# Optimization experiments

Measured on AMD Instinct MI355X. Metric: run time of the kernel, lower is better.

## Reference

```python
import jax, jax.numpy as jnp
import numpy as np

EMBED_DIM = 1024
NUM_HEADS = 16
HEAD_DIM = EMBED_DIM // NUM_HEADS
EXPANSION = 4
EPS = 1e-5


def setup_inputs() -> dict:
    key = jax.random.key(0)
    ks = jax.random.split(key, 8)
    D, F = EMBED_DIM, EMBED_DIM * EXPANSION
    s = lambda d: 1.0 / np.sqrt(d)
    return {
        "x": jax.random.normal(ks[0], (8, 1024, D), jnp.float32),
        "qkv_w": jax.random.normal(ks[1], (D, 3 * D), jnp.float32) * s(D),
        "qkv_b": jnp.zeros((3 * D,), jnp.float32),
        "out_w": jax.random.normal(ks[2], (D, D), jnp.float32) * s(D),
        "out_b": jnp.zeros((D,), jnp.float32),
        "ffn_w1": jax.random.normal(ks[3], (D, F), jnp.float32) * s(D),
        "ffn_b1": jnp.zeros((F,), jnp.float32),
        "ffn_w2": jax.random.normal(ks[4], (F, D), jnp.float32) * s(F),
        "ffn_b2": jnp.zeros((D,), jnp.float32),
        "ln1_g": jnp.ones((D,), jnp.float32),
        "ln1_b": jnp.zeros((D,), jnp.float32),
        "ln2_g": jnp.ones((D,), jnp.float32),
        "ln2_b": jnp.zeros((D,), jnp.float32),
    }


def _layernorm(x, g, b):
    mu = jnp.mean(x, axis=-1, keepdims=True)
    var = jnp.mean(jnp.square(x - mu), axis=-1, keepdims=True)
    return (x - mu) * jax.lax.rsqrt(var + EPS) * g + b


def reference(x, qkv_w, qkv_b, out_w, out_b, ffn_w1, ffn_b1, ffn_w2, ffn_b2,
              ln1_g, ln1_b, ln2_g, ln2_b):
    B, N, D = x.shape
    H, Hd = NUM_HEADS, HEAD_DIM
    scale = Hd ** -0.5

    residual = x
    h = _layernorm(x, ln1_g, ln1_b)
    qkv = h @ qkv_w + qkv_b                      # [B, N, 3D]
    q, k, v = jnp.split(qkv, 3, axis=-1)
    # [B, N, D] -> [B, H, N, Hd]
    reshape = lambda t: t.reshape(B, N, H, Hd).transpose(0, 2, 1, 3)
    q, k, v = reshape(q), reshape(k), reshape(v)

    attn = jnp.einsum("bhnd,bhmd->bhnm", q, k) * scale
    attn = jax.nn.softmax(attn, axis=-1)
    o = jnp.einsum("bhnm,bhmd->bhnd", attn, v)   # [B, H, N, Hd]
    o = o.transpose(0, 2, 1, 3).reshape(B, N, D)
    o = o @ out_w + out_b
    x = residual + o

    residual = x
    h = _layernorm(x, ln2_g, ln2_b)
    h = jax.nn.gelu(h @ ffn_w1 + ffn_b1, approximate=False) @ ffn_w2 + ffn_b2
    return residual + h
```

## Files before the change

kernel.cpp:

```cpp
#include <hip/hip_runtime.h>
#include <hip/hip_bf16.h>


typedef float f32x4 __attribute__((ext_vector_type(4)));
typedef float f32x16 __attribute__((ext_vector_type(16)));
typedef short bf16x8 __attribute__((ext_vector_type(8)));

#define DEV __device__ __forceinline__

DEV f32x4 mfma16(bf16x8 a, bf16x8 b, f32x4 c) {
    return __builtin_amdgcn_mfma_f32_16x16x32_bf16(a, b, c, 0, 0, 0);
}

DEV f32x16 mfma32(bf16x8 a, bf16x8 b, f32x16 c) {
    return __builtin_amdgcn_mfma_f32_32x32x16_bf16(a, b, c, 0, 0, 0);
}

DEV ushort f2bf(float f) {
    union { float f; unsigned u; } v; v.f = f;
    unsigned r = v.u + 0x7FFFu + ((v.u >> 16) & 1u);
    return (ushort)(r >> 16);
}

DEV unsigned cvtpk(float lo, float hi) {
    unsigned r;
    asm("v_cvt_pk_bf16_f32 %0, %1, %2" : "=v"(r) : "v"(lo), "v"(hi));
    return r;
}

DEV void gload_lds16(const void* g, void* l) {
    __builtin_amdgcn_global_load_lds(
        (const __attribute__((address_space(1))) void*)g,
        (__attribute__((address_space(3))) void*)l, 16, 0, 0);
}

template <int N> DEV void vmwait() {
    asm volatile("s_waitcnt vmcnt(%0)" :: "n"(N) : "memory");
}
DEV void lgkm0() {
    asm volatile("s_waitcnt lgkmcnt(0)" ::: "memory");
}

__global__ __launch_bounds__(256) void transpose_w(
    const float* __restrict__ src, ushort* __restrict__ dst, int K, int N)
{
    __shared__ float tile[32][33];
    const int n0 = blockIdx.x * 32, k0 = blockIdx.y * 32;
    const int tx = threadIdx.x, ty = threadIdx.y;
#pragma unroll
    for (int i = 0; i < 32; i += 8)
        tile[ty + i][tx] = src[(size_t)(k0 + ty + i) * N + n0 + tx];
    __syncthreads();
#pragma unroll
    for (int i = 0; i < 32; i += 8)
        dst[(size_t)(n0 + ty + i) * K + k0 + tx] = f2bf(tile[tx][ty + i]);
}

__global__ __launch_bounds__(256) void transpose_v(
    const ushort* __restrict__ qkvb, ushort* __restrict__ vt)
{
    __shared__ ushort tile[32][33];
    const int b = blockIdx.z >> 4, h = blockIdx.z & 15;
    const int n0 = blockIdx.x * 32, d0 = blockIdx.y * 32;
    const int tx = threadIdx.x, ty = threadIdx.y;
#pragma unroll
    for (int i = 0; i < 32; i += 8)
        tile[ty + i][tx] =
            qkvb[(size_t)(b * 1024 + n0 + ty + i) * 3072 + 2048 + h * 64 + d0 + tx];
    __syncthreads();
#pragma unroll
    for (int i = 0; i < 32; i += 8)
        vt[((size_t)(b * 16 + h) * 64 + d0 + ty + i) * 1024 + n0 + tx] = tile[tx][ty + i];
}

__global__ __launch_bounds__(256) void ln_bf16(
    const float* __restrict__ x, const float* __restrict__ gw,
    const float* __restrict__ bw, ushort* __restrict__ out)
{
    const int row = blockIdx.x;
    const int t = threadIdx.x;
    const float4 v = ((const float4*)(x + (size_t)row * 1024))[t];
    float s  = v.x + v.y + v.z + v.w;
    float s2 = v.x * v.x + v.y * v.y + v.z * v.z + v.w * v.w;
#pragma unroll
    for (int off = 32; off; off >>= 1) {
        s  += __shfl_xor(s, off);
        s2 += __shfl_xor(s2, off);
    }
    __shared__ float red[16];
    const int wave = t >> 6, lane = t & 63;
    if (lane == 0) { red[wave] = s; red[8 + wave] = s2; }
    __syncthreads();
    s  = red[0] + red[1] + red[2] + red[3];
    s2 = red[8] + red[9] + red[10] + red[11];
    const float mean = s * (1.0f / 1024.0f);
    const float var  = s2 * (1.0f / 1024.0f) - mean * mean;
    const float rstd = rsqrtf(var + 1e-5f);
    const float4 gv = ((const float4*)gw)[t];
    const float4 bv = ((const float4*)bw)[t];
    ushort4 o;
    o.x = f2bf((v.x - mean) * rstd * gv.x + bv.x);
    o.y = f2bf((v.y - mean) * rstd * gv.y + bv.y);
    o.z = f2bf((v.z - mean) * rstd * gv.z + bv.z);
    o.w = f2bf((v.w - mean) * rstd * gv.w + bv.w);
    ((ushort4*)out)[(size_t)row * 256 + t] = o;
}

template <int BM, int BN, int WM_, int WN_, int EPI>
__global__ __launch_bounds__(512, 2) void gemm4p(
    const ushort* __restrict__ A, const ushort* __restrict__ BT,
    const float* __restrict__ bias, const float* __restrict__ res,
    void* __restrict__ out, int M, int N, int K)
{
    constexpr int BK = 64;
    constexpr int MR = BM / WM_ / 16;
    constexpr int NR = BN / WN_ / 16;
    constexpr int MH = MR / 2;
    constexpr int CM = MH / 2;
    constexpr int LA = (BM / 2) / 64;
    constexpr int LB = (BN / 2) / 64;
    constexpr int VMN = LA + LB;
    constexpr int ABYTES = BM * BK * 2;
    constexpr int BBYTES = BN * BK * 2;

    extern __shared__ __align__(16) char smem[];
#define ASB(b) (smem + (b) * ABYTES)
#define BSB(b) (smem + 2 * ABYTES + (b) * BBYTES)

    const int tid = threadIdx.x;
    const int wave = tid >> 6, lane = tid & 63;
    const int g = lane >> 4, lr = lane & 15;
    const int wr = wave / WN_, wc = wave % WN_;
    const int akey = (lr & 7) << 4;

    const int gx = gridDim.x;
    const int nwg = gx * gridDim.y;
    int id = blockIdx.y * gx + blockIdx.x;
    id = (id & 7) * (nwg >> 3) + (id >> 3);
    const int m0 = (id / gx) * BM, n0 = (id % gx) * BN;

    const int trow = tid >> 3;
    const int tblk = (tid & 7) ^ (trow & 7);
    const ushort* pA = A  + (size_t)(m0 + trow) * K + tblk * 8;
    const ushort* pB = BT + (size_t)(n0 + trow) * K + tblk * 8;
    const int woff = wave * 1024;

#define STAGE_A(b, h, kt) do { \
    _Pragma("unroll") for (int i = 0; i < LA; ++i) \
        gload_lds16(pA + ((size_t)((h) * (BM / 2) + i * 64)) * K + (size_t)(kt) * 64, \
                    ASB(b) + (h) * (BM / 2) * 128 + i * 8192 + woff); \
} while (0)
#define STAGE_B(b, h, kt) do { \
    _Pragma("unroll") for (int i = 0; i < LB; ++i) \
        gload_lds16(pB + ((size_t)((h) * (BN / 2) + i * 64)) * K + (size_t)(kt) * 64, \
                    BSB(b) + (h) * (BN / 2) * 128 + i * 8192 + woff); \
} while (0)

    bf16x8 af[CM][2], bfr[NR][2];
    f32x4 acc[MR][NR] = {};

#define LOAD_A(b, h, cj) do { \
    const char* rb_ = ASB(b) + ((h) * (BM / 2) + wr * ((BM / 2) / WM_) \
                               + (cj) * CM * 16 + lr) * 128; \
    _Pragma("unroll") for (int cm = 0; cm < CM; ++cm) \
    _Pragma("unroll") for (int kk = 0; kk < 2; ++kk) \
        af[cm][kk] = *(const bf16x8*)(rb_ + cm * 2048 + ((kk * 64 + g * 16) ^ akey)); \
} while (0)
#define LOAD_B(b) do { \
    const char* rb_ = BSB(b) + (wc * (BN / WN_) + lr) * 128; \
    _Pragma("unroll") for (int ni = 0; ni < NR; ++ni) \
    _Pragma("unroll") for (int kk = 0; kk < 2; ++kk) \
        bfr[ni][kk] = *(const bf16x8*)(rb_ + ni * 2048 + ((kk * 64 + g * 16) ^ akey)); \
} while (0)
#define MFMA_PH(h, cj) do { \
    __builtin_amdgcn_s_setprio(1); \
    _Pragma("unroll") for (int cm = 0; cm < CM; ++cm) \
    _Pragma("unroll") for (int ni = 0; ni < NR; ++ni) \
    _Pragma("unroll") for (int kk = 0; kk < 2; ++kk) \
        acc[(h) * MH + (cj) * CM + cm][ni] = \
            mfma16(af[cm][kk], bfr[ni][kk], acc[(h) * MH + (cj) * CM + cm][ni]); \
    __builtin_amdgcn_s_setprio(0); \
} while (0)

    const int NT = K >> 6;

    STAGE_A(0, 0, 0); STAGE_A(0, 1, 0); STAGE_B(0, 0, 0); STAGE_B(0, 1, 0);
    STAGE_B(1, 0, 1);
    STAGE_A(1, 0, 1);
    vmwait<VMN>();
    __builtin_amdgcn_s_barrier();

    for (int kt = 0; kt < NT; ++kt) {
        const int b = kt & 1, nb = b ^ 1;
        LOAD_A(b, 0, 0); LOAD_B(b);
        if (kt + 1 < NT) STAGE_B(nb, 1, kt + 1);
        __builtin_amdgcn_s_barrier(); lgkm0();
        MFMA_PH(0, 0);
        LOAD_A(b, 0, 1);
        if (kt + 1 < NT) STAGE_A(nb, 1, kt + 1);
        __builtin_amdgcn_s_barrier(); lgkm0();
        MFMA_PH(0, 1);
        LOAD_A(b, 1, 0);
        if (kt + 2 < NT) STAGE_B(b, 0, kt + 2);
        __builtin_amdgcn_s_barrier(); lgkm0();
        MFMA_PH(1, 0);
        LOAD_A(b, 1, 1);
        if (kt + 2 < NT) { STAGE_A(b, 0, kt + 2); vmwait<VMN>(); }
        else if (kt + 1 < NT) vmwait<0>();
        __builtin_amdgcn_s_barrier(); lgkm0();
        MFMA_PH(1, 1);
    }

#pragma unroll
    for (int mi = 0; mi < MR; ++mi) {
        const int row0 = m0 + (mi / MH) * (BM / 2) + wr * ((BM / 2) / WM_)
                       + (mi % MH) * 16 + 4 * g;
#pragma unroll
        for (int ni = 0; ni < NR; ++ni) {
            const int col = n0 + wc * (BN / WN_) + ni * 16 + lr;
            const float bv = bias[col];
#pragma unroll
            for (int r = 0; r < 4; ++r) {
                float v = acc[mi][ni][r] + bv;
                const size_t idx = (size_t)(row0 + r) * N + col;
                if constexpr (EPI == 1) {
                    ((float*)out)[idx] = v + res[idx];
                } else if constexpr (EPI == 2) {
                    const float u = 1.595769122f * v + 0.071354816f * v * v * v;
                    const float gs = 1.0f / (1.0f + __expf(-u));
                    ((ushort*)out)[idx] = f2bf(v * gs);
                } else {
                    ((ushort*)out)[idx] = f2bf(v);
                }
            }
        }
    }
#undef STAGE_A
#undef STAGE_B
#undef LOAD_A
#undef LOAD_B
#undef MFMA_PH
#undef ASB
#undef BSB
}

__global__ __launch_bounds__(256) void attn_kernel(
    const ushort* __restrict__ qkv, const ushort* __restrict__ vtb,
    ushort* __restrict__ o)
{
    __shared__ __align__(16) ushort Ks[64 * 64];
    __shared__ __align__(16) ushort Vt[64 * 64];

    const int tid = threadIdx.x;
    const int wave = tid >> 6, lane = tid & 63;
    const int lq = lane & 31;
    const int hi = lane >> 5;
    const int l7 = lane & 7;

    const int hwid = blockIdx.x;
    const int logical = (hwid & 7) * 128 + (hwid >> 3);
    const int bh = logical >> 3, qt = logical & 7;
    const int b = bh >> 4, head = bh & 15;
    const int q0 = qt * 128 + wave * 32;

    const size_t base  = (size_t)b * 1024 * 3072;
    const size_t vbase = (size_t)bh * 64 * 1024;

    union BF8 { bf16x8 v; ushort u[8]; unsigned w[4]; };

    BF8 qf[4];
    {
        const ushort* qrow = qkv + base + (size_t)(q0 + lq) * 3072 + head * 64;
#pragma unroll
        for (int s = 0; s < 4; ++s) {
            *(ushort4*)&qf[s].u[0] = *(const ushort4*)(qrow + 16 * s + 4 * hi);
            *(ushort4*)&qf[s].u[4] = *(const ushort4*)(qrow + 16 * s + 8 + 4 * hi);
        }
    }

    const int sr = tid >> 3, sc = tid & 7;
    const int swz = (sc ^ (sr & 7)) << 3;
    const ushort* kg0 = qkv + base + (size_t)sr * 3072 + 1024 + head * 64 + sc * 8;
    const ushort* kg1 = kg0 + (size_t)32 * 3072;
    const ushort* vg0 = vtb + vbase + (size_t)sr * 1024 + sc * 8;
    const ushort* vg1 = vg0 + (size_t)32 * 1024;
    ushort* ksw0 = Ks + sr * 64 + swz;
    ushort* ksw1 = Ks + (sr + 32) * 64 + swz;
    ushort* vsw0 = Vt + sr * 64 + swz;
    ushort* vsw1 = Vt + (sr + 32) * 64 + swz;

    float m_st = -1e30f, l_st = 0.f;
    f32x16 oacc[2] = {};

    constexpr float SCL = 0.18033688011112042f;

    for (int kt = 0; kt < 16; ++kt) {
        const int n0 = kt * 64;
        __syncthreads();
        *(bf16x8*)ksw0 = *(const bf16x8*)(kg0 + (size_t)n0 * 3072);
        *(bf16x8*)ksw1 = *(const bf16x8*)(kg1 + (size_t)n0 * 3072);
        *(bf16x8*)vsw0 = *(const bf16x8*)(vg0 + n0);
        *(bf16x8*)vsw1 = *(const bf16x8*)(vg1 + n0);
        __syncthreads();

        f32x16 sacc[2];
#pragma unroll
        for (int kb = 0; kb < 2; ++kb) {
            f32x16 a = {};
            const ushort* krow = Ks + (kb * 32 + lq) * 64;
#pragma unroll
            for (int s = 0; s < 4; ++s) {
                BF8 kf;
                *(ushort4*)&kf.u[0] = *(const ushort4*)(krow + (((2 * s)     ^ l7) << 3) + 4 * hi);
                *(ushort4*)&kf.u[4] = *(const ushort4*)(krow + (((2 * s + 1) ^ l7) << 3) + 4 * hi);
                a = mfma32(kf.v, qf[s].v, a);
            }
            sacc[kb] = a;
        }

        float mloc = -1e30f;
#pragma unroll
        for (int kb = 0; kb < 2; ++kb)
#pragma unroll
            for (int r = 0; r < 16; ++r)
                mloc = fmaxf(mloc, sacc[kb][r]);
        mloc = fmaxf(mloc, __shfl_xor(mloc, 32));
        const float mnew = fmaxf(m_st, mloc * SCL);
        const float resc = exp2f(m_st - mnew);
        m_st = mnew;

        float psum = 0.f;
#pragma unroll
        for (int kb = 0; kb < 2; ++kb)
#pragma unroll
            for (int r = 0; r < 16; ++r) {
                const float pe = exp2f(fmaf(sacc[kb][r], SCL, -mnew));
                sacc[kb][r] = pe;
                psum += pe;
            }
        psum += __shfl_xor(psum, 32);
        l_st = l_st * resc + psum;
#pragma unroll
        for (int nb = 0; nb < 2; ++nb)
#pragma unroll
            for (int r = 0; r < 16; ++r)
                oacc[nb][r] *= resc;

#pragma unroll
        for (int kb = 0; kb < 2; ++kb) {
            BF8 pf[2];
#pragma unroll
            for (int t = 0; t < 2; ++t)
#pragma unroll
                for (int w = 0; w < 4; ++w)
                    pf[t].w[w] = cvtpk(sacc[kb][8 * t + 2 * w], sacc[kb][8 * t + 2 * w + 1]);
#pragma unroll
            for (int nb = 0; nb < 2; ++nb) {
                const ushort* vrow = Vt + (nb * 32 + lq) * 64;
#pragma unroll
                for (int t = 0; t < 2; ++t) {
                    BF8 vf;
                    const int blk = 4 * kb + 2 * t;
                    *(ushort4*)&vf.u[0] = *(const ushort4*)(vrow + ((blk       ^ l7) << 3) + 4 * hi);
                    *(ushort4*)&vf.u[4] = *(const ushort4*)(vrow + (((blk + 1) ^ l7) << 3) + 4 * hi);
                    oacc[nb] = mfma32(vf.v, pf[t].v, oacc[nb]);
                }
            }
        }
    }

    const float inv = 1.0f / l_st;
    ushort* orow = o + (size_t)(b * 1024 + q0 + lq) * 1024 + head * 64;
#pragma unroll
    for (int nb = 0; nb < 2; ++nb)
#pragma unroll
        for (int u = 0; u < 4; ++u) {
            uint2 wv;
            wv.x = cvtpk(oacc[nb][4 * u] * inv,     oacc[nb][4 * u + 1] * inv);
            wv.y = cvtpk(oacc[nb][4 * u + 2] * inv, oacc[nb][4 * u + 3] * inv);
            *(uint2*)(orow + nb * 32 + 8 * u + 4 * hi) = wv;
        }
}

extern "C" void kernel_launch(void* const* d_in, const int* in_sizes, int n_in,
                              void* d_out, int out_size, void* d_ws, size_t ws_size,
                              hipStream_t stream)
{
    const float* x      = (const float*)d_in[0];
    const float* qkv_w  = (const float*)d_in[1];
    const float* qkv_b  = (const float*)d_in[2];
    const float* out_w  = (const float*)d_in[3];
    const float* out_b  = (const float*)d_in[4];
    const float* ffn_w1 = (const float*)d_in[5];
    const float* ffn_b1 = (const float*)d_in[6];
    const float* ffn_w2 = (const float*)d_in[7];
    const float* ffn_b2 = (const float*)d_in[8];
    const float* ln1_g  = (const float*)d_in[9];
    const float* ln1_b  = (const float*)d_in[10];
    const float* ln2_g  = (const float*)d_in[11];
    const float* ln2_b  = (const float*)d_in[12];

    constexpr size_t MB = 1u << 20;
    char* ws = (char*)d_ws;
    ushort* wt_qkv = (ushort*)(ws + 0 * MB);
    ushort* wt_out = (ushort*)(ws + 6 * MB);
    ushort* wt_f1  = (ushort*)(ws + 8 * MB);
    ushort* wt_f2  = (ushort*)(ws + 16 * MB);
    float*  x1     = (float*) (ws + 24 * MB);
    ushort* vtb    = (ushort*)(ws + 24 * MB);
    ushort* hbuf   = (ushort*)(ws + 56 * MB);
    ushort* qkvb   = (ushort*)(ws + 72 * MB);
    ushort* obuf   = (ushort*)(ws + 120 * MB);
    ushort* gbuf   = (ushort*)(ws + 72 * MB);

    const dim3 tb(32, 8);
    transpose_w<<<dim3(3072 / 32, 1024 / 32), tb, 0, stream>>>(qkv_w,  wt_qkv, 1024, 3072);
    transpose_w<<<dim3(1024 / 32, 1024 / 32), tb, 0, stream>>>(out_w,  wt_out, 1024, 1024);
    transpose_w<<<dim3(4096 / 32, 1024 / 32), tb, 0, stream>>>(ffn_w1, wt_f1,  1024, 4096);
    transpose_w<<<dim3(1024 / 32, 4096 / 32), tb, 0, stream>>>(ffn_w2, wt_f2,  4096, 1024);

    ln_bf16<<<8192, 256, 0, stream>>>(x, ln1_g, ln1_b, hbuf);

    constexpr int LDS_256 = (256 + 256) * 64 * 2 * 2;
    constexpr int LDS_128 = (256 + 128) * 64 * 2 * 2;

    gemm4p<256, 256, 2, 4, 0><<<dim3(12, 32), 512, LDS_256, stream>>>(
        hbuf, wt_qkv, qkv_b, nullptr, qkvb, 8192, 3072, 1024);

    transpose_v<<<dim3(32, 2, 128), tb, 0, stream>>>(qkvb, vtb);

    attn_kernel<<<1024, 256, 0, stream>>>(qkvb, vtb, obuf);

    gemm4p<256, 128, 4, 2, 1><<<dim3(8, 32), 512, LDS_128, stream>>>(
        obuf, wt_out, out_b, x, x1, 8192, 1024, 1024);

    ln_bf16<<<8192, 256, 0, stream>>>(x1, ln2_g, ln2_b, hbuf);

    gemm4p<256, 256, 2, 4, 2><<<dim3(16, 32), 512, LDS_256, stream>>>(
        hbuf, wt_f1, ffn_b1, nullptr, gbuf, 8192, 4096, 1024);

    gemm4p<256, 128, 4, 2, 1><<<dim3(8, 32), 512, LDS_128, stream>>>(
        gbuf, wt_f2, ffn_b2, x1, (float*)d_out, 8192, 1024, 4096);
}
```

Baseline: 352.2 us.

## Prefetch next K/V tile into registers and skip rescale when max stable

The attention loop now loads the next K/V tile from global memory into registers while computing on the current tile in LDS, hiding global load latency behind the MFMA work. It also adds a lazy online-softmax rescale that updates the running max and rescales the accumulators only when some lane's new max exceeds the stored max by more than 8 (log2 domain), so most iterations avoid the rescale multiplies. This raises register pressure and lets exponent values grow up to 2^8 before rescaling, a bounded precision risk. It relies on an lgkm0 helper and raw barriers instead of __syncthreads.

```diff
diff --git a/kernel.cpp b/kernel.cpp
--- a/kernel.cpp
+++ b/kernel.cpp
@@ -294,14 +294,26 @@
 
     constexpr float SCL = 0.18033688011112042f;
 
+    bf16x8 rk0 = *(const bf16x8*)kg0;
+    bf16x8 rk1 = *(const bf16x8*)kg1;
+    bf16x8 rv0 = *(const bf16x8*)vg0;
+    bf16x8 rv1 = *(const bf16x8*)vg1;
+
     for (int kt = 0; kt < 16; ++kt) {
-        const int n0 = kt * 64;
-        __syncthreads();
-        *(bf16x8*)ksw0 = *(const bf16x8*)(kg0 + (size_t)n0 * 3072);
-        *(bf16x8*)ksw1 = *(const bf16x8*)(kg1 + (size_t)n0 * 3072);
-        *(bf16x8*)vsw0 = *(const bf16x8*)(vg0 + n0);
-        *(bf16x8*)vsw1 = *(const bf16x8*)(vg1 + n0);
-        __syncthreads();
+        *(bf16x8*)ksw0 = rk0;
+        *(bf16x8*)ksw1 = rk1;
+        *(bf16x8*)vsw0 = rv0;
+        *(bf16x8*)vsw1 = rv1;
+        lgkm0();
+        __builtin_amdgcn_s_barrier();
+
+        if (kt + 1 < 16) {
+            const size_t n1 = (size_t)(kt + 1) * 64;
+            rk0 = *(const bf16x8*)(kg0 + n1 * 3072);
+            rk1 = *(const bf16x8*)(kg1 + n1 * 3072);
+            rv0 = *(const bf16x8*)(vg0 + n1);
+            rv1 = *(const bf16x8*)(vg1 + n1);
+        }
 
         f32x16 sacc[2];
 #pragma unroll
@@ -325,26 +337,30 @@
             for (int r = 0; r < 16; ++r)
                 mloc = fmaxf(mloc, sacc[kb][r]);
         mloc = fmaxf(mloc, __shfl_xor(mloc, 32));
-        const float mnew = fmaxf(m_st, mloc * SCL);
-        const float resc = exp2f(m_st - mnew);
-        m_st = mnew;
+        const float mxs = mloc * SCL;
+        if (!__all(mxs <= m_st + 8.0f)) {
+            const float mnew = fmaxf(m_st, mxs);
+            const float resc = exp2f(m_st - mnew);
+            m_st = mnew;
+            l_st *= resc;
+#pragma unroll
+            for (int nb = 0; nb < 2; ++nb)
+#pragma unroll
+                for (int r = 0; r < 16; ++r)
+                    oacc[nb][r] *= resc;
+        }
 
         float psum = 0.f;
 #pragma unroll
         for (int kb = 0; kb < 2; ++kb)
 #pragma unroll
             for (int r = 0; r < 16; ++r) {
-                const float pe = exp2f(fmaf(sacc[kb][r], SCL, -mnew));
+                const float pe = exp2f(fmaf(sacc[kb][r], SCL, -m_st));
                 sacc[kb][r] = pe;
                 psum += pe;
             }
         psum += __shfl_xor(psum, 32);
-        l_st = l_st * resc + psum;
-#pragma unroll
-        for (int nb = 0; nb < 2; ++nb)
-#pragma unroll
-            for (int r = 0; r < 16; ++r)
-                oacc[nb][r] *= resc;
+        l_st += psum;
 
 #pragma unroll
         for (int kb = 0; kb < 2; ++kb) {
@@ -367,6 +383,9 @@
                 }
             }
         }
+
+        lgkm0();
+        __builtin_amdgcn_s_barrier();
     }
 
     const float inv = 1.0f / l_st;
```

Measured after the change: 353.3 us. About the same (+0.3%).
